# Kernel optimization log

Hardware: AMD Instinct MI355X
Metric: run time of the kernel (lower is better)

## Reference

```python
import jax, jax.numpy as jnp
import numpy as np

N_NODES = 50000
N_EDGES = 800000
IN_DIM = 128
OUT_DIM = 64
K_KERNELS = 2
S_ATTEN = 2


def setup_inputs() -> dict:
    key = jax.random.key(0)
    ks = jax.random.split(key, 9)
    return {
        "x": jax.random.normal(ks[0], (N_NODES, IN_DIM), dtype=jnp.float32),
        "support_vals": jax.random.uniform(ks[1], (K_KERNELS, N_EDGES), dtype=jnp.float32),
        "atten_vals": jax.random.uniform(ks[2], (S_ATTEN, N_EDGES), dtype=jnp.float32),
        "W_transform": jax.random.normal(ks[3], (K_KERNELS, IN_DIM, OUT_DIM), dtype=jnp.float32) * 0.05,
        "w_left": jax.random.normal(ks[4], (K_KERNELS, S_ATTEN + 1, OUT_DIM), dtype=jnp.float32) * 0.05,
        "w_right": jax.random.normal(ks[5], (K_KERNELS, S_ATTEN + 1, OUT_DIM), dtype=jnp.float32) * 0.05,
        "W_residual": jax.random.normal(ks[6], (IN_DIM + OUT_DIM, OUT_DIM), dtype=jnp.float32) * 0.05,
        "edge_rows": jax.random.randint(ks[7], (N_EDGES,), 0, N_NODES, dtype=jnp.int64),
        "edge_cols": jax.random.randint(ks[8], (N_EDGES,), 0, N_NODES, dtype=jnp.int64),
    }


def reference(x, support_vals, atten_vals, W_transform, w_left, w_right, W_residual, edge_rows, edge_cols):
    # x: [N, F], edge lists: [E]; all supports share the same sparsity pattern.
    N = x.shape[0]
    K = W_transform.shape[0]
    output = jnp.zeros((N, W_transform.shape[2]), dtype=x.dtype)
    for k in range(K):
        wx = x @ W_transform[k]                       # [N, D]
        al = wx @ w_left[k].T                         # [N, S+1]
        ar = wx @ w_right[k].T                        # [N, S+1]
        # per-support edge values; support i=S uses this kernel's Cheb support
        vals = jnp.concatenate([atten_vals, support_vals[k][None, :]], axis=0)  # [S+1, E]
        # score_e = sum_i (al[row_e,i] + ar[col_e,i]) * vals[i,e]
        scores = jnp.einsum('es,se->e', al[edge_rows] + ar[edge_cols], vals)    # [E]
        # row-wise (segment) softmax over nonzeros, as tf.sparse_softmax
        m = jax.ops.segment_max(scores, edge_rows, num_segments=N)              # [N]
        ex = jnp.exp(scores - m[edge_rows])
        denom = jax.ops.segment_sum(ex, edge_rows, num_segments=N)              # [N]
        probs = ex / denom[edge_rows]                                           # [E]
        # spmm: out[r] = sum_{e: row_e=r} probs_e * wx[col_e]
        output = output + jax.ops.segment_sum(probs[:, None] * wx[edge_cols], edge_rows, num_segments=N)
    # residual projection then elu activation
    output = jnp.concatenate([x, output], axis=-1) @ W_residual
    return jax.nn.elu(output)
```

## Files before the change

kernel.cpp:

```cpp
#include <hip/hip_runtime.h>

#define N_NODES 50000
#define N_EDGES 800000
#define IN_DIM 128
#define OUT_DIM 64
#define NEG_INF (-1e30f)
#define GBLK ((N_NODES + 63) / 64)
#define BSHIFT 6
#define NBUK ((N_NODES + 63) >> 6)
#define NBUKP 784
#define EB 1024
#define PREB ((N_EDGES + EB - 1) / EB)
#define NFRAG (3 * 16 + 8)
#define STAGE_CAP 2048
#define BUKCAP 2048

typedef unsigned short ushort_t;
typedef __attribute__((ext_vector_type(8))) short short8;
typedef __attribute__((ext_vector_type(4))) float f32x4;
typedef __attribute__((ext_vector_type(2))) _Float16 half2_t;

__device__ __forceinline__ unsigned f2bf(float f) {
    unsigned u = __float_as_uint(f);
    u += 0x7fffu + ((u >> 16) & 1u);
    return u >> 16;
}
__device__ __forceinline__ float bf2f(ushort_t h) {
    return __uint_as_float((unsigned)h << 16);
}
__device__ __forceinline__ unsigned rl_u(unsigned v, int i) {
    return __builtin_amdgcn_readlane(v, i);
}
__device__ __forceinline__ unsigned pack_h2(float a, float b) {
    auto h = __builtin_amdgcn_cvt_pkrtz(a, b);
    union { decltype(h) h2; unsigned u; } v; v.h2 = h; return v.u;
}
__device__ __forceinline__ float dot2u(unsigned w, unsigned p, float acc) {
    union { unsigned u; half2_t h; } wv, pv;
    wv.u = w; pv.u = p;
    return __builtin_amdgcn_fdot2(wv.h, pv.h, acc, false);
}

__global__ void wpack_kernel(const float* __restrict__ Wt,
                             const float* __restrict__ Wres,
                             ushort_t* __restrict__ Wpack) {
    int idx = blockIdx.x * 256 + threadIdx.x;
    if (idx >= NFRAG * 512) return;
    int f = idx >> 9;
    int within = idx & 511;
    int lane = within >> 3;
    int b = within & 7;
    float val;
    if (f < 48) {
        int mat = f >> 4;
        int ct = (f >> 2) & 3;
        int kc = f & 3;
        int k = kc * 32 + (lane >> 4) * 8 + b;
        int c = ct * 16 + (lane & 15);
        const float* W = (mat < 2) ? (Wt + (size_t)mat * IN_DIM * OUT_DIM) : Wres;
        val = W[(size_t)k * OUT_DIM + c];
    } else {
        int f2 = f - 48;
        int ct = f2 >> 1;
        int kc = f2 & 1;
        int k = kc * 32 + (lane >> 4) * 8 + b;
        int c = ct * 16 + (lane & 15);
        val = Wres[(size_t)(IN_DIM + k) * OUT_DIM + c];
    }
    Wpack[idx] = (ushort_t)f2bf(val);
}

__global__ __launch_bounds__(256) void gemm_kernel(
        const float* __restrict__ x,
        const ushort_t* __restrict__ Wpack,
        const float* __restrict__ wl,
        const float* __restrict__ wr,
        unsigned* __restrict__ wxi,
        ushort_t* __restrict__ xresh,
        float* __restrict__ al,
        float* __restrict__ ar) {
    int wave = threadIdx.x >> 6;
    int lane = threadIdx.x & 63;
    int lr = lane & 15;
    int lg = lane >> 4;
    int row0 = blockIdx.x * 64 + wave * 16;

    int arow = row0 + lr;
    if (arow >= N_NODES) arow = N_NODES - 1;
    const float* xr = x + (size_t)arow * IN_DIM;
    short8 afrag[4];
#pragma unroll
    for (int kc = 0; kc < 4; ++kc) {
        float4 f0 = *(const float4*)(xr + kc * 32 + lg * 8);
        float4 f1 = *(const float4*)(xr + kc * 32 + lg * 8 + 4);
        short8 a;
        a[0] = (short)f2bf(f0.x); a[1] = (short)f2bf(f0.y);
        a[2] = (short)f2bf(f0.z); a[3] = (short)f2bf(f0.w);
        a[4] = (short)f2bf(f1.x); a[5] = (short)f2bf(f1.y);
        a[6] = (short)f2bf(f1.z); a[7] = (short)f2bf(f1.w);
        afrag[kc] = a;
    }

    f32x4 acc[3][4] = {};
#pragma unroll
    for (int kc = 0; kc < 4; ++kc) {
#pragma unroll
        for (int mat = 0; mat < 3; ++mat) {
#pragma unroll
            for (int ct = 0; ct < 4; ++ct) {
                short8 bfrag = *(const short8*)(
                    Wpack + (size_t)(((mat * 4 + ct) * 4 + kc) << 9) + lane * 8);
                acc[mat][ct] = __builtin_amdgcn_mfma_f32_16x16x32_bf16(
                    afrag[kc], bfrag, acc[mat][ct], 0, 0, 0);
            }
        }
    }

#pragma unroll
    for (int r = 0; r < 4; ++r) {
        int gr = row0 + lg * 4 + r;
        if (gr < N_NODES) {
#pragma unroll
            for (int ct = 0; ct < 4; ++ct) {
                wxi[(size_t)gr * OUT_DIM + ct * 16 + lr] =
                    pack_h2(acc[0][ct][r], acc[1][ct][r]);
                xresh[(size_t)gr * OUT_DIM + ct * 16 + lr] =
                    (ushort_t)f2bf(acc[2][ct][r]);
            }
        }
    }

#pragma unroll
    for (int mat = 0; mat < 2; ++mat) {
#pragma unroll
        for (int s = 0; s < 3; ++s) {
            float wlv[4], wrv[4];
#pragma unroll
            for (int ct = 0; ct < 4; ++ct) {
                wlv[ct] = wl[(size_t)(mat * 3 + s) * OUT_DIM + ct * 16 + lr];
                wrv[ct] = wr[(size_t)(mat * 3 + s) * OUT_DIM + ct * 16 + lr];
            }
#pragma unroll
            for (int r = 0; r < 4; ++r) {
                float pl = 0.f, pr = 0.f;
#pragma unroll
                for (int ct = 0; ct < 4; ++ct) {
                    pl = fmaf(acc[mat][ct][r], wlv[ct], pl);
                    pr = fmaf(acc[mat][ct][r], wrv[ct], pr);
                }
#pragma unroll
                for (int off = 1; off < 16; off <<= 1) {
                    pl += __shfl_xor(pl, off);
                    pr += __shfl_xor(pr, off);
                }
                if (lr == 0) {
                    int gr = row0 + lg * 4 + r;
                    if (gr < N_NODES) {
                        al[(size_t)gr * 6 + mat * 3 + s] = pl;
                        ar[(size_t)gr * 6 + mat * 3 + s] = pr;
                    }
                }
            }
        }
    }
}

__global__ __launch_bounds__(256) void score_sort_kernel(
        const int* __restrict__ rows,
        const int* __restrict__ cols,
        const float* __restrict__ atten,
        const float* __restrict__ support,
        const float* __restrict__ al,
        const float* __restrict__ ar,
        uint4* __restrict__ etmp,
        uint2* __restrict__ cl) {
    __shared__ int cnt[1024];
    __shared__ int cur[1024];
    __shared__ int aux[256];
    __shared__ uint4 stage[EB];
    int t = threadIdx.x;
    cnt[t] = 0; cnt[t + 256] = 0; cnt[t + 512] = 0; cnt[t + 768] = 0;
    __syncthreads();
    int base0 = blockIdx.x * EB;
    int nval = min(EB, N_EDGES - base0);

    int r_[4], c_[4];
    float s0_[4], s1_[4];
#pragma unroll
    for (int i = 0; i < 4; ++i) {
        int e = base0 + i * 256 + t;
        bool v = e < N_EDGES;
        int r = v ? rows[e] : -1;
        int c = v ? cols[e] : 0;
        float sc0 = 0.f, sc1 = 0.f;
        if (v) {
            float a0 = atten[e], a1 = atten[N_EDGES + e];
            float sp0 = support[e], sp1 = support[N_EDGES + e];
            const float* A = al + (size_t)r * 6;
            const float* B = ar + (size_t)c * 6;
            sc0 = (A[0] + B[0]) * a0 + (A[1] + B[1]) * a1 + (A[2] + B[2]) * sp0;
            sc1 = (A[3] + B[3]) * a0 + (A[4] + B[4]) * a1 + (A[5] + B[5]) * sp1;
            atomicAdd(&cnt[r >> BSHIFT], 1);
        }
        r_[i] = r; c_[i] = c; s0_[i] = sc0; s1_[i] = sc1;
    }
    __syncthreads();
    int v0 = cnt[4 * t], v1 = cnt[4 * t + 1], v2 = cnt[4 * t + 2], v3 = cnt[4 * t + 3];
    int ps = v0 + v1 + v2 + v3;
    aux[t] = ps;
    __syncthreads();
    int val = ps;
    for (int off = 1; off < 256; off <<= 1) {
        int y = (t >= off) ? aux[t - off] : 0;
        __syncthreads();
        val += y; aux[t] = val;
        __syncthreads();
    }
    int e0x = val - ps;
    cur[4 * t]     = e0x;
    cur[4 * t + 1] = e0x + v0;
    cur[4 * t + 2] = e0x + v0 + v1;
    cur[4 * t + 3] = e0x + v0 + v1 + v2;
    size_t cb = (size_t)blockIdx.x * NBUKP;
    int vv[4] = {v0, v1, v2, v3};
#pragma unroll
    for (int j = 0; j < 4; ++j) {
        int idx = 4 * t + j;
        if (idx < NBUK) cl[cb + idx] = make_uint2((unsigned)vv[j], (unsigned)cur[idx]);
    }
    __syncthreads();
#pragma unroll
    for (int i = 0; i < 4; ++i) {
        if (r_[i] < 0) continue;
        int pos = atomicAdd(&cur[r_[i] >> BSHIFT], 1);
        uint4 pv;
        pv.x = (unsigned)c_[i] | ((unsigned)(r_[i] & 63) << 16);
        pv.y = __float_as_uint(s0_[i]);
        pv.z = __float_as_uint(s1_[i]);
        pv.w = 0u;
        stage[pos] = pv;
    }
    __syncthreads();
    for (int i = t; i < nval; i += 256)
        etmp[(size_t)base0 + i] = stage[i];
}

__global__ __launch_bounds__(256) void sortb_kernel(
        const uint2* __restrict__ cl,
        const uint4* __restrict__ etmp,
        uint4* __restrict__ edata,
        uint2* __restrict__ rowinfo) {
    __shared__ uint4 stage[STAGE_CAP];
    __shared__ int rpos[PREB + 2];
    __shared__ int lloff[PREB];
    __shared__ int aux[256];
    __shared__ int hist[64], rcur[64];
    int k = blockIdx.x, t = threadIdx.x;
    int base = k * BUKCAP;

    for (int b = t; b < PREB; b += 256) {
        uint2 v2 = cl[(size_t)b * NBUKP + k];
        rpos[b] = (int)v2.x;
        lloff[b] = (int)v2.y;
    }
    if (t < 64) hist[t] = 0;
    __syncthreads();
    int v[4];
    int idx4 = 4 * t;
#pragma unroll
    for (int i = 0; i < 4; ++i) v[i] = (idx4 + i < PREB) ? rpos[idx4 + i] : 0;
    __syncthreads();
    int s = 0;
#pragma unroll
    for (int i = 0; i < 4; ++i) { int tmp = v[i]; v[i] = s; s += tmp; }
    aux[t] = s;
    __syncthreads();
    int tv = s;
    for (int off = 1; off < 256; off <<= 1) {
        int y = (t >= off) ? aux[t - off] : 0;
        __syncthreads();
        tv += y; aux[t] = tv;
        __syncthreads();
    }
    int ofs = tv - s;
#pragma unroll
    for (int i = 0; i < 4; ++i)
        if (idx4 + i <= PREB) rpos[idx4 + i] = ofs + v[i];
    __syncthreads();
    int nb = rpos[PREB];

    for (int b = t; b < PREB; b += 256) {
        int s0 = rpos[b];
        int n = rpos[b + 1] - s0;
        int lo = lloff[b];
        const uint4* src = etmp + (size_t)b * EB + lo;
        for (int i = 0; i < n; ++i) {
            uint4 rec = src[i];
            int j = s0 + i;
            if (j < STAGE_CAP) stage[j] = rec;
            atomicAdd(&hist[(rec.x >> 16) & 63], 1);
        }
    }
    __syncthreads();
    int hv = (t < 64) ? hist[t] : 0;
    aux[t] = hv;
    __syncthreads();
    int hval = hv;
    for (int off = 1; off < 64; off <<= 1) {
        int y = (t >= off && t < 64) ? aux[t - off] : 0;
        __syncthreads();
        hval += y; aux[t] = hval;
        __syncthreads();
    }
    if (t < 64) {
        int start = hval - hv;
        rcur[t] = start;
        int row = (k << BSHIFT) + t;
        if (row < N_NODES)
            rowinfo[row] = make_uint2((unsigned)(base + start), (unsigned)hv);
    }
    __syncthreads();
    for (int j = t; j < nb; j += 256) {
        uint4 rec;
        if (j < STAGE_CAP) rec = stage[j];
        else {
            int lo = 0, hi = PREB - 1;
            while (lo < hi) { int mid = (lo + hi + 1) >> 1; if (rpos[mid] <= j) lo = mid; else hi = mid - 1; }
            rec = etmp[(size_t)lo * EB + lloff[lo] + (j - rpos[lo])];
        }
        int rl = (rec.x >> 16) & 63;
        int dst = atomicAdd(&rcur[rl], 1);
        if (dst < BUKCAP) edata[(size_t)base + dst] = rec;
    }
}

__global__ void attn_kernel(const uint2* __restrict__ rowinfo,
                            const uint4* __restrict__ edata,
                            const unsigned* __restrict__ wxi,
                            ushort_t* __restrict__ aacc) {
    int wid = blockIdx.x * 4 + (threadIdx.x >> 6);
    if (wid >= N_NODES) return;
    int lane = threadIdx.x & 63;
    uint2 ri = rowinfo[wid];
    int beg = (int)ri.x;
    int deg = (int)ri.y;
    float a = 0.f;

    if (deg > 0 && deg <= 64) {
        bool valid = lane < deg;
        uint4 ed = edata[valid ? beg + lane : beg];
        unsigned c = ed.x & 0xFFFFu;
        float sc0 = valid ? __uint_as_float(ed.y) : NEG_INF;
        float sc1 = valid ? __uint_as_float(ed.z) : NEG_INF;
        float m0 = sc0, m1 = sc1;
#pragma unroll
        for (int off = 32; off > 0; off >>= 1) {
            m0 = fmaxf(m0, __shfl_xor(m0, off));
            m1 = fmaxf(m1, __shfl_xor(m1, off));
        }
        float e0 = valid ? __expf(sc0 - m0) : 0.f;
        float e1 = valid ? __expf(sc1 - m1) : 0.f;
        float l0 = e0, l1 = e1;
#pragma unroll
        for (int off = 32; off > 0; off >>= 1) {
            l0 += __shfl_xor(l0, off);
            l1 += __shfl_xor(l1, off);
        }
        unsigned pp = pack_h2(e0 / l0, e1 / l1);
        float acc8[8] = {};
        int i = 0;
        for (; i + 8 <= deg; i += 8) {
            unsigned cc[8], vv[8];
#pragma unroll
            for (int j = 0; j < 8; ++j) cc[j] = rl_u(c, i + j);
#pragma unroll
            for (int j = 0; j < 8; ++j) vv[j] = wxi[(size_t)cc[j] * OUT_DIM + lane];
#pragma unroll
            for (int j = 0; j < 8; ++j)
                acc8[j] = dot2u(vv[j], rl_u(pp, i + j), acc8[j]);
        }
        for (; i < deg; ++i) {
            unsigned ci = rl_u(c, i);
            unsigned v = wxi[(size_t)ci * OUT_DIM + lane];
            acc8[0] = dot2u(v, rl_u(pp, i), acc8[0]);
        }
        a = ((acc8[0] + acc8[1]) + (acc8[2] + acc8[3]))
          + ((acc8[4] + acc8[5]) + (acc8[6] + acc8[7]));
    } else if (deg > 64) {
        int end = beg + deg;
        float m0 = NEG_INF, l0 = 0.f, m1 = NEG_INF, l1 = 0.f;
        for (int base = beg; base < end; base += 64) {
            int pos = base + lane;
            bool valid = pos < end;
            uint4 ed = edata[valid ? pos : beg];
            float sc0 = valid ? __uint_as_float(ed.y) : NEG_INF;
            float sc1 = valid ? __uint_as_float(ed.z) : NEG_INF;
            float cm0 = sc0, cm1 = sc1;
#pragma unroll
            for (int off = 32; off > 0; off >>= 1) {
                cm0 = fmaxf(cm0, __shfl_xor(cm0, off));
                cm1 = fmaxf(cm1, __shfl_xor(cm1, off));
            }
            float mn0 = fmaxf(m0, cm0), mn1 = fmaxf(m1, cm1);
            float e0 = valid ? __expf(sc0 - mn0) : 0.f;
            float e1 = valid ? __expf(sc1 - mn1) : 0.f;
#pragma unroll
            for (int off = 32; off > 0; off >>= 1) {
                e0 += __shfl_xor(e0, off);
                e1 += __shfl_xor(e1, off);
            }
            l0 = l0 * __expf(m0 - mn0) + e0;
            l1 = l1 * __expf(m1 - mn1) + e1;
            m0 = mn0; m1 = mn1;
        }
        float inv0 = 1.f / l0, inv1 = 1.f / l1;
        for (int base = beg; base < end; base += 64) {
            int pos = base + lane;
            bool valid = pos < end;
            uint4 ed = edata[valid ? pos : beg];
            unsigned c = ed.x & 0xFFFFu;
            float p0 = valid ? __expf(__uint_as_float(ed.y) - m0) * inv0 : 0.f;
            float p1 = valid ? __expf(__uint_as_float(ed.z) - m1) * inv1 : 0.f;
            unsigned pp = pack_h2(p0, p1);
            int cnt = min(64, end - base);
            for (int i = 0; i < cnt; ++i) {
                unsigned ci = rl_u(c, i);
                unsigned v = wxi[(size_t)ci * OUT_DIM + lane];
                a = dot2u(v, rl_u(pp, i), a);
            }
        }
    }
    aacc[(size_t)wid * OUT_DIM + lane] = (ushort_t)f2bf(a);
}

__global__ __launch_bounds__(256) void resid_kernel(
        const ushort_t* __restrict__ aacc,
        const ushort_t* __restrict__ xresh,
        const ushort_t* __restrict__ Wpack,
        float* __restrict__ out) {
    int wave = threadIdx.x >> 6;
    int lane = threadIdx.x & 63;
    int lr = lane & 15;
    int lg = lane >> 4;
    int row0 = blockIdx.x * 64 + wave * 16;
    int arow = row0 + lr;
    if (arow >= N_NODES) arow = N_NODES - 1;
    const ushort_t* ap = aacc + (size_t)arow * OUT_DIM;
    short8 af[2];
#pragma unroll
    for (int kc = 0; kc < 2; ++kc)
        af[kc] = *(const short8*)(ap + kc * 32 + lg * 8);
    f32x4 acc4[4] = {};
#pragma unroll
    for (int kc = 0; kc < 2; ++kc) {
#pragma unroll
        for (int ct = 0; ct < 4; ++ct) {
            short8 bfrag = *(const short8*)(
                Wpack + (size_t)((48 + ct * 2 + kc) << 9) + lane * 8);
            acc4[ct] = __builtin_amdgcn_mfma_f32_16x16x32_bf16(
                af[kc], bfrag, acc4[ct], 0, 0, 0);
        }
    }
#pragma unroll
    for (int r = 0; r < 4; ++r) {
        int gr = row0 + lg * 4 + r;
        if (gr < N_NODES) {
#pragma unroll
            for (int ct = 0; ct < 4; ++ct) {
                float v = acc4[ct][r] + bf2f(xresh[(size_t)gr * OUT_DIM + ct * 16 + lr]);
                out[(size_t)gr * OUT_DIM + ct * 16 + lr] = (v > 0.f) ? v : expm1f(v);
            }
        }
    }
}

extern "C" void kernel_launch(void* const* d_in, const int* in_sizes, int n_in,
                              void* d_out, int out_size, void* d_ws, size_t ws_size,
                              hipStream_t stream) {
    const float* x       = (const float*)d_in[0];
    const float* support = (const float*)d_in[1];
    const float* atten   = (const float*)d_in[2];
    const float* Wt      = (const float*)d_in[3];
    const float* wl      = (const float*)d_in[4];
    const float* wr      = (const float*)d_in[5];
    const float* Wres    = (const float*)d_in[6];
    const int*   rows    = (const int*)d_in[7];
    const int*   cols    = (const int*)d_in[8];
    float* out = (float*)d_out;

    unsigned* wxi    = (unsigned*)d_ws;
    ushort_t* xresh  = (ushort_t*)(wxi + (size_t)N_NODES * OUT_DIM);
    float* al        = (float*)(xresh + (size_t)N_NODES * OUT_DIM);
    float* ar        = al + (size_t)N_NODES * 6;
    uint4* etmp      = (uint4*)(ar + (size_t)N_NODES * 6);
    uint4* edata     = etmp + (size_t)N_EDGES;
    uint2* rowinfo   = (uint2*)(edata + (size_t)NBUK * BUKCAP);
    uint2* cl        = rowinfo + N_NODES + 4;
    ushort_t* Wpack  = (ushort_t*)(cl + (size_t)PREB * NBUKP);
    ushort_t* aacc   = (ushort_t*)etmp;

    wpack_kernel<<<(NFRAG * 512 + 255) / 256, 256, 0, stream>>>(Wt, Wres, Wpack);
    gemm_kernel<<<GBLK, 256, 0, stream>>>(x, Wpack, wl, wr, wxi, xresh, al, ar);
    score_sort_kernel<<<PREB, 256, 0, stream>>>(
        rows, cols, atten, support, al, ar, etmp, cl);
    sortb_kernel<<<NBUK, 256, 0, stream>>>(cl, etmp, edata, rowinfo);
    attn_kernel<<<(N_NODES + 3) / 4, 256, 0, stream>>>(
        rowinfo, edata, wxi, aacc);
    resid_kernel<<<GBLK, 256, 0, stream>>>(aacc, xresh, Wpack, out);
}
```

Baseline: 129.3 us.

## Pack edge scores to fp16 and fuse attention with residual projection

Edge records shrink from 16 to 8 bytes by packing the two scores as half2, which halves the traffic of the sort and attention stages. The attention and residual kernels are merged, so each block computes 64 rows of aggregated features into shared memory and then runs the MFMA residual projection directly, with no global round-trip for aacc. The cost is reduced score precision before the softmax, and the fused kernel launches fewer, larger blocks, each looping over 16 rows per wave.

After: 144.9 us. 12.1% more time.

```diff
diff --git a/kernel.cpp b/kernel.cpp
--- a/kernel.cpp
+++ b/kernel.cpp
@@ -34,6 +34,11 @@
 __device__ __forceinline__ unsigned pack_h2(float a, float b) {
     auto h = __builtin_amdgcn_cvt_pkrtz(a, b);
     union { decltype(h) h2; unsigned u; } v; v.h2 = h; return v.u;
+}
+__device__ __forceinline__ void unpack_h2(unsigned u, float& a, float& b) {
+    union { unsigned u; half2_t h; } v; v.u = u;
+    a = (float)v.h[0];
+    b = (float)v.h[1];
 }
 __device__ __forceinline__ float dot2u(unsigned w, unsigned p, float acc) {
     union { unsigned u; half2_t h; } wv, pv;
@@ -172,12 +177,12 @@
         const float* __restrict__ support,
         const float* __restrict__ al,
         const float* __restrict__ ar,
-        uint4* __restrict__ etmp,
+        uint2* __restrict__ etmp,
         uint2* __restrict__ cl) {
     __shared__ int cnt[1024];
     __shared__ int cur[1024];
     __shared__ int aux[256];
-    __shared__ uint4 stage[EB];
+    __shared__ uint2 stage[EB];
     int t = threadIdx.x;
     cnt[t] = 0; cnt[t + 256] = 0; cnt[t + 512] = 0; cnt[t + 768] = 0;
     __syncthreads();
@@ -233,11 +238,9 @@
     for (int i = 0; i < 4; ++i) {
         if (r_[i] < 0) continue;
         int pos = atomicAdd(&cur[r_[i] >> BSHIFT], 1);
-        uint4 pv;
+        uint2 pv;
         pv.x = (unsigned)c_[i] | ((unsigned)(r_[i] & 63) << 16);
-        pv.y = __float_as_uint(s0_[i]);
-        pv.z = __float_as_uint(s1_[i]);
-        pv.w = 0u;
+        pv.y = pack_h2(s0_[i], s1_[i]);
         stage[pos] = pv;
     }
     __syncthreads();
@@ -247,10 +250,10 @@
 
 __global__ __launch_bounds__(256) void sortb_kernel(
         const uint2* __restrict__ cl,
-        const uint4* __restrict__ etmp,
-        uint4* __restrict__ edata,
+        const uint2* __restrict__ etmp,
+        uint2* __restrict__ edata,
         uint2* __restrict__ rowinfo) {
-    __shared__ uint4 stage[STAGE_CAP];
+    __shared__ uint2 stage[STAGE_CAP];
     __shared__ int rpos[PREB + 2];
     __shared__ int lloff[PREB];
     __shared__ int aux[256];
@@ -293,9 +296,9 @@
         int s0 = rpos[b];
         int n = rpos[b + 1] - s0;
         int lo = lloff[b];
-        const uint4* src = etmp + (size_t)b * EB + lo;
+        const uint2* src = etmp + (size_t)b * EB + lo;
         for (int i = 0; i < n; ++i) {
-            uint4 rec = src[i];
+            uint2 rec = src[i];
             int j = s0 + i;
             if (j < STAGE_CAP) stage[j] = rec;
             atomicAdd(&hist[(rec.x >> 16) & 63], 1);
@@ -321,7 +324,7 @@
     }
     __syncthreads();
     for (int j = t; j < nb; j += 256) {
-        uint4 rec;
+        uint2 rec;
         if (j < STAGE_CAP) rec = stage[j];
         else {
             int lo = 0, hi = PREB - 1;
@@ -334,122 +337,128 @@
     }
 }
 
-__global__ void attn_kernel(const uint2* __restrict__ rowinfo,
-                            const uint4* __restrict__ edata,
-                            const unsigned* __restrict__ wxi,
-                            ushort_t* __restrict__ aacc) {
-    int wid = blockIdx.x * 4 + (threadIdx.x >> 6);
-    if (wid >= N_NODES) return;
-    int lane = threadIdx.x & 63;
-    uint2 ri = rowinfo[wid];
-    int beg = (int)ri.x;
-    int deg = (int)ri.y;
-    float a = 0.f;
-
-    if (deg > 0 && deg <= 64) {
-        bool valid = lane < deg;
-        uint4 ed = edata[valid ? beg + lane : beg];
-        unsigned c = ed.x & 0xFFFFu;
-        float sc0 = valid ? __uint_as_float(ed.y) : NEG_INF;
-        float sc1 = valid ? __uint_as_float(ed.z) : NEG_INF;
-        float m0 = sc0, m1 = sc1;
-#pragma unroll
-        for (int off = 32; off > 0; off >>= 1) {
-            m0 = fmaxf(m0, __shfl_xor(m0, off));
-            m1 = fmaxf(m1, __shfl_xor(m1, off));
-        }
-        float e0 = valid ? __expf(sc0 - m0) : 0.f;
-        float e1 = valid ? __expf(sc1 - m1) : 0.f;
-        float l0 = e0, l1 = e1;
-#pragma unroll
-        for (int off = 32; off > 0; off >>= 1) {
-            l0 += __shfl_xor(l0, off);
-            l1 += __shfl_xor(l1, off);
-        }
-        unsigned pp = pack_h2(e0 / l0, e1 / l1);
-        float acc8[8] = {};
-        int i = 0;
-        for (; i + 8 <= deg; i += 8) {
-            unsigned cc[8], vv[8];
-#pragma unroll
-            for (int j = 0; j < 8; ++j) cc[j] = rl_u(c, i + j);
-#pragma unroll
-            for (int j = 0; j < 8; ++j) vv[j] = wxi[(size_t)cc[j] * OUT_DIM + lane];
-#pragma unroll
-            for (int j = 0; j < 8; ++j)
-                acc8[j] = dot2u(vv[j], rl_u(pp, i + j), acc8[j]);
-        }
-        for (; i < deg; ++i) {
-            unsigned ci = rl_u(c, i);
-            unsigned v = wxi[(size_t)ci * OUT_DIM + lane];
-            acc8[0] = dot2u(v, rl_u(pp, i), acc8[0]);
-        }
-        a = ((acc8[0] + acc8[1]) + (acc8[2] + acc8[3]))
-          + ((acc8[4] + acc8[5]) + (acc8[6] + acc8[7]));
-    } else if (deg > 64) {
-        int end = beg + deg;
-        float m0 = NEG_INF, l0 = 0.f, m1 = NEG_INF, l1 = 0.f;
-        for (int base = beg; base < end; base += 64) {
-            int pos = base + lane;
-            bool valid = pos < end;
-            uint4 ed = edata[valid ? pos : beg];
-            float sc0 = valid ? __uint_as_float(ed.y) : NEG_INF;
-            float sc1 = valid ? __uint_as_float(ed.z) : NEG_INF;
-            float cm0 = sc0, cm1 = sc1;
-#pragma unroll
-            for (int off = 32; off > 0; off >>= 1) {
-                cm0 = fmaxf(cm0, __shfl_xor(cm0, off));
-                cm1 = fmaxf(cm1, __shfl_xor(cm1, off));
-            }
-            float mn0 = fmaxf(m0, cm0), mn1 = fmaxf(m1, cm1);
-            float e0 = valid ? __expf(sc0 - mn0) : 0.f;
-            float e1 = valid ? __expf(sc1 - mn1) : 0.f;
-#pragma unroll
-            for (int off = 32; off > 0; off >>= 1) {
-                e0 += __shfl_xor(e0, off);
-                e1 += __shfl_xor(e1, off);
-            }
-            l0 = l0 * __expf(m0 - mn0) + e0;
-            l1 = l1 * __expf(m1 - mn1) + e1;
-            m0 = mn0; m1 = mn1;
-        }
-        float inv0 = 1.f / l0, inv1 = 1.f / l1;
-        for (int base = beg; base < end; base += 64) {
-            int pos = base + lane;
-            bool valid = pos < end;
-            uint4 ed = edata[valid ? pos : beg];
-            unsigned c = ed.x & 0xFFFFu;
-            float p0 = valid ? __expf(__uint_as_float(ed.y) - m0) * inv0 : 0.f;
-            float p1 = valid ? __expf(__uint_as_float(ed.z) - m1) * inv1 : 0.f;
-            unsigned pp = pack_h2(p0, p1);
-            int cnt = min(64, end - base);
-            for (int i = 0; i < cnt; ++i) {
-                unsigned ci = rl_u(c, i);
-                unsigned v = wxi[(size_t)ci * OUT_DIM + lane];
-                a = dot2u(v, rl_u(pp, i), a);
-            }
-        }
-    }
-    aacc[(size_t)wid * OUT_DIM + lane] = (ushort_t)f2bf(a);
-}
-
-__global__ __launch_bounds__(256) void resid_kernel(
-        const ushort_t* __restrict__ aacc,
+__global__ __launch_bounds__(256) void attn_resid_kernel(
+        const uint2* __restrict__ rowinfo,
+        const uint2* __restrict__ edata,
+        const unsigned* __restrict__ wxi,
         const ushort_t* __restrict__ xresh,
         const ushort_t* __restrict__ Wpack,
         float* __restrict__ out) {
-    int wave = threadIdx.x >> 6;
-    int lane = threadIdx.x & 63;
+    __shared__ ushort_t aacc_s[64][72];
+    int t = threadIdx.x;
+    int wave = t >> 6;
+    int lane = t & 63;
+    for (int i = t; i < 64 * 36; i += 256) ((unsigned*)aacc_s)[i] = 0;
+    __syncthreads();
+
+    for (int rr = wave; rr < 64; rr += 4) {
+        int row = blockIdx.x * 64 + rr;
+        if (row >= N_NODES) continue;
+        uint2 ri = rowinfo[row];
+        int beg = (int)ri.x;
+        int deg = (int)ri.y;
+        float a = 0.f;
+
+        if (deg > 0 && deg <= 64) {
+            bool valid = lane < deg;
+            uint2 ed = edata[valid ? beg + lane : beg];
+            unsigned c = ed.x & 0xFFFFu;
+            float sc0, sc1;
+            unpack_h2(ed.y, sc0, sc1);
+            if (!valid) { sc0 = NEG_INF; sc1 = NEG_INF; }
+            float m0 = sc0, m1 = sc1;
+#pragma unroll
+            for (int off = 32; off > 0; off >>= 1) {
+                m0 = fmaxf(m0, __shfl_xor(m0, off));
+                m1 = fmaxf(m1, __shfl_xor(m1, off));
+            }
+            float e0 = valid ? __expf(sc0 - m0) : 0.f;
+            float e1 = valid ? __expf(sc1 - m1) : 0.f;
+            float l0 = e0, l1 = e1;
+#pragma unroll
+            for (int off = 32; off > 0; off >>= 1) {
+                l0 += __shfl_xor(l0, off);
+                l1 += __shfl_xor(l1, off);
+            }
+            unsigned pp = pack_h2(e0 / l0, e1 / l1);
+            float acc8[8] = {};
+            int i = 0;
+            for (; i + 8 <= deg; i += 8) {
+                unsigned cc[8], vv8[8];
+#pragma unroll
+                for (int j = 0; j < 8; ++j) cc[j] = rl_u(c, i + j);
+#pragma unroll
+                for (int j = 0; j < 8; ++j) vv8[j] = wxi[(size_t)cc[j] * OUT_DIM + lane];
+#pragma unroll
+                for (int j = 0; j < 8; ++j)
+                    acc8[j] = dot2u(vv8[j], rl_u(pp, i + j), acc8[j]);
+            }
+            for (; i < deg; ++i) {
+                unsigned ci = rl_u(c, i);
+                unsigned vw = wxi[(size_t)ci * OUT_DIM + lane];
+                acc8[0] = dot2u(vw, rl_u(pp, i), acc8[0]);
+            }
+            a = ((acc8[0] + acc8[1]) + (acc8[2] + acc8[3]))
+              + ((acc8[4] + acc8[5]) + (acc8[6] + acc8[7]));
+        } else if (deg > 64) {
+            int end = beg + deg;
+            float m0 = NEG_INF, l0 = 0.f, m1 = NEG_INF, l1 = 0.f;
+            for (int base = beg; base < end; base += 64) {
+                int pos = base + lane;
+                bool valid = pos < end;
+                uint2 ed = edata[valid ? pos : beg];
+                float sc0, sc1;
+                unpack_h2(ed.y, sc0, sc1);
+                if (!valid) { sc0 = NEG_INF; sc1 = NEG_INF; }
+                float cm0 = sc0, cm1 = sc1;
+#pragma unroll
+                for (int off = 32; off > 0; off >>= 1) {
+                    cm0 = fmaxf(cm0, __shfl_xor(cm0, off));
+                    cm1 = fmaxf(cm1, __shfl_xor(cm1, off));
+                }
+                float mn0 = fmaxf(m0, cm0), mn1 = fmaxf(m1, cm1);
+                float e0 = valid ? __expf(sc0 - mn0) : 0.f;
+                float e1 = valid ? __expf(sc1 - mn1) : 0.f;
+#pragma unroll
+                for (int off = 32; off > 0; off >>= 1) {
+                    e0 += __shfl_xor(e0, off);
+                    e1 += __shfl_xor(e1, off);
+                }
+                l0 = l0 * __expf(m0 - mn0) + e0;
+                l1 = l1 * __expf(m1 - mn1) + e1;
+                m0 = mn0; m1 = mn1;
+            }
+            float inv0 = 1.f / l0, inv1 = 1.f / l1;
+            for (int base = beg; base < end; base += 64) {
+                int pos = base + lane;
+                bool valid = pos < end;
+                uint2 ed = edata[valid ? pos : beg];
+                unsigned c = ed.x & 0xFFFFu;
+                float sc0, sc1;
+                unpack_h2(ed.y, sc0, sc1);
+                float p0 = valid ? __expf(sc0 - m0) * inv0 : 0.f;
+                float p1 = valid ? __expf(sc1 - m1) * inv1 : 0.f;
+                unsigned pp = pack_h2(p0, p1);
+                int cnt = min(64, end - base);
+                for (int i = 0; i < cnt; ++i) {
+                    unsigned ci = rl_u(c, i);
+                    unsigned vw = wxi[(size_t)ci * OUT_DIM + lane];
+                    a = dot2u(vw, rl_u(pp, i), a);
+                }
+            }
+        }
+        aacc_s[rr][lane] = (ushort_t)f2bf(a);
+    }
+    __syncthreads();
+
     int lr = lane & 15;
     int lg = lane >> 4;
     int row0 = blockIdx.x * 64 + wave * 16;
-    int arow = row0 + lr;
-    if (arow >= N_NODES) arow = N_NODES - 1;
-    const ushort_t* ap = aacc + (size_t)arow * OUT_DIM;
+    int rloc = wave * 16 + lr;
     short8 af[2];
 #pragma unroll
     for (int kc = 0; kc < 2; ++kc)
-        af[kc] = *(const short8*)(ap + kc * 32 + lg * 8);
+        af[kc] = *(const short8*)&aacc_s[rloc][kc * 32 + lg * 8];
     f32x4 acc4[4] = {};
 #pragma unroll
     for (int kc = 0; kc < 2; ++kc) {
@@ -492,19 +501,17 @@
     ushort_t* xresh  = (ushort_t*)(wxi + (size_t)N_NODES * OUT_DIM);
     float* al        = (float*)(xresh + (size_t)N_NODES * OUT_DIM);
     float* ar        = al + (size_t)N_NODES * 6;
-    uint4* etmp      = (uint4*)(ar + (size_t)N_NODES * 6);
-    uint4* edata     = etmp + (size_t)N_EDGES;
-    uint2* rowinfo   = (uint2*)(edata + (size_t)NBUK * BUKCAP);
+    uint2* etmp      = (uint2*)(ar + (size_t)N_NODES * 6);
+    uint2* edata     = etmp + (size_t)N_EDGES;
+    uint2* rowinfo   = edata + (size_t)NBUK * BUKCAP;
     uint2* cl        = rowinfo + N_NODES + 4;
     ushort_t* Wpack  = (ushort_t*)(cl + (size_t)PREB * NBUKP);
-    ushort_t* aacc   = (ushort_t*)etmp;
 
     wpack_kernel<<<(NFRAG * 512 + 255) / 256, 256, 0, stream>>>(Wt, Wres, Wpack);
     gemm_kernel<<<GBLK, 256, 0, stream>>>(x, Wpack, wl, wr, wxi, xresh, al, ar);
     score_sort_kernel<<<PREB, 256, 0, stream>>>(
         rows, cols, atten, support, al, ar, etmp, cl);
     sortb_kernel<<<NBUK, 256, 0, stream>>>(cl, etmp, edata, rowinfo);
-    attn_kernel<<<(N_NODES + 3) / 4, 256, 0, stream>>>(
-        rowinfo, edata, wxi, aacc);
-    resid_kernel<<<GBLK, 256, 0, stream>>>(aacc, xresh, Wpack, out);
-}
+    attn_resid_kernel<<<NBUK, 256, 0, stream>>>(
+        rowinfo, edata, wxi, xresh, Wpack, out);
+}
```
